# Performance work log

Measured on AMD Instinct MI355X. Metric: run time of the kernel, lower is better.

## Reference

```python
import jax, jax.numpy as jnp
import numpy as np

DEPTH = 4
EPS = 1e-05


def _hard_sigmoid(x):
    # Keras hard_sigmoid: clip(0.2*x + 0.5, 0, 1)
    return jnp.clip(0.2 * x + 0.5, 0.0, 1.0)


def _ln(x, gamma, beta):
    m = jnp.mean(x, axis=-1, keepdims=True)
    std = jnp.sqrt(jnp.var(x, axis=-1, keepdims=True) + EPS)
    return gamma * ((x - m) / (std + EPS)) + beta


def setup_inputs() -> dict:
    key = jax.random.key(0)
    ks = jax.random.split(key, 4)
    B, T, Din, H = 64, 256, 512, 512
    D = Din + H
    O = 2 * H + Din
    x = jax.random.normal(ks[0], (B, T, Din), dtype=jnp.float32)
    mask = jnp.ones((B, T), dtype=bool)
    W = jax.random.normal(ks[1], (D, O), dtype=jnp.float32) * (1.0 / np.sqrt(D))
    U = jax.random.normal(ks[2], (D, O), dtype=jnp.float32) * (1.0 / np.sqrt(D))
    b = jnp.zeros((O,), dtype=jnp.float32)
    gammas = jnp.ones((2, O), dtype=jnp.float32)
    betas = jnp.zeros((2, O), dtype=jnp.float32)
    return {"x": x, "mask": mask, "W": W, "U": U, "b": b,
            "gammas": gammas, "betas": betas, "bucket_size": 256}


def _forward(x, mask, W, U, b, gammas, betas, bucket_size):
    B, T, Din = x.shape
    D = W.shape[0]            # Din + H
    H = W.shape[1] - D        # hidden_dim
    # pad x with zeros in the hidden slots: (B,T,D) -> time-major (Tb,B,D)
    xp = jnp.concatenate([x, jnp.zeros((B, T, H), x.dtype)], axis=-1)
    xs = jnp.transpose(xp, (1, 0, 2))[:bucket_size]           # (Tb,B,D)
    m = jnp.transpose(mask, (1, 0))[:bucket_size]             # (Tb,B) bool
    # mask2 = mask * (1 - shift_left(mask)) : marks the last valid position
    m_shift = jnp.concatenate([m[1:], jnp.zeros((1, B), bool)], axis=0)
    m2 = jnp.logical_and(m, jnp.logical_not(m_shift))          # (Tb,B)
    mf = m.astype(x.dtype)[:, :, None]                         # (Tb,B,1)
    m2f = m2[:, :, None]                                       # (Tb,B,1) bool

    g0, g1 = gammas[0], gammas[1]
    be0, be1 = betas[0], betas[1]

    def hstep(carry, inp):
        h_tm1, fk_tm1 = carry
        xt, fkp, mt, m2t = inp
        sum1 = _ln(xt @ W, g0, be0)
        sum2 = _ln(h_tm1 @ U, g1, be1)
        total = sum1 + sum2 + b
        fk_c = _hard_sigmoid(total[:, :D])                     # (B,D)
        h_ = jnp.tanh(total[:, D:])                            # (B,H)
        h_pad = jnp.concatenate([jnp.zeros((xt.shape[0], D - H), xt.dtype), h_], axis=-1)
        h_cand = (1.0 - fk_c) * xt + fk_c * h_pad
        h = fkp * h_tm1 + (1.0 - fkp) * h_cand
        fk = fkp + (1.0 - fkp) * fk_c
        fk = jnp.where(m2t, 0.0, fk)
        out_h = mt * h + (1.0 - mt) * h_tm1
        out_fk = mt * fk + (1.0 - mt) * fk_tm1
        return (out_h, out_fk), (out_h, out_fk)

    Tb = xs.shape[0]
    fk_prev = jnp.zeros((Tb, B, D), x.dtype)
    h_seq = xs
    for _ in range(DEPTH):
        init = (jnp.zeros((B, D), x.dtype), jnp.zeros((B, D), x.dtype))
        _, (h_seq, fk_seq) = jax.lax.scan(hstep, init, (h_seq, fk_prev, mf, m2f))
        fk_prev = jnp.concatenate([fk_seq[1:], jnp.zeros((1, B, D), x.dtype)], axis=0)
    # outputs = last depth, last timestep, hidden slice
    return h_seq[-1, :, Din:]                                  # (B,H)


def reference(x, mask, W, U, b, gammas, betas, bucket_size):
    return _forward(x, mask, W, U, b, gammas, betas, bucket_size)
```

## Files before the change

### kernel.cpp

```cpp
#include <hip/hip_runtime.h>
#include <hip/hip_bf16.h>
#include <math.h>

#define B_   64
#define T_   256
#define DIN_ 512
#define H_   512
#define D_   1024
#define O_   1536
#define TB_  (T_*B_)
#define EPSf 1e-5f
#define NWG  96
#define NSLOT (T_ + 6)

typedef short  bf16x8 __attribute__((ext_vector_type(8)));
typedef float  f32x4  __attribute__((ext_vector_type(4)));
typedef ushort u16x4  __attribute__((ext_vector_type(4)));
typedef unsigned long long ull;

#define SPLIT1(f, Hm, Lm) { __hip_bfloat16 _h = __float2bfloat16(f); (Hm) = *(ushort*)&_h; \
    __hip_bfloat16 _l = __float2bfloat16((f) - __bfloat162float(_h)); (Lm) = *(ushort*)&_l; }

__device__ inline void st_f32_coh(float* p, float v) {
    __hip_atomic_store(p, v, __ATOMIC_RELAXED, __HIP_MEMORY_SCOPE_AGENT);
}
__device__ inline void st_u16_coh(ushort* p, ushort v) {
    __hip_atomic_store(p, v, __ATOMIC_RELAXED, __HIP_MEMORY_SCOPE_AGENT);
}
__device__ inline void st_u32_coh(unsigned* p, unsigned v) {
    __hip_atomic_store(p, v, __ATOMIC_RELAXED, __HIP_MEMORY_SCOPE_AGENT);
}
__device__ inline void st_f32x2_coh(float* p, float a, float b) {
    union { float f[2]; ull u; } pk;
    pk.f[0] = a; pk.f[1] = b;
    __hip_atomic_store((ull*)p, pk.u, __ATOMIC_RELAXED, __HIP_MEMORY_SCOPE_AGENT);
}

__global__ __launch_bounds__(256) void k_mask(const int* __restrict__ mask,
                                              int* __restrict__ mcode) {
    int g = blockIdx.x * 256 + threadIdx.x;
    int t = g >> 6, b = g & 63;
    int mt = mask[b * T_ + t] != 0;
    int mn = (t + 1 < T_) ? (mask[b * T_ + t + 1] != 0) : 0;
    mcode[g] = mt | (mn << 1);
}

__global__ __launch_bounds__(256) void k_prepx(const float* __restrict__ x,
                                               ushort* __restrict__ Xh) {
    int g  = blockIdx.x * 256 + threadIdx.x;
    int i4 = g * 4;
    int row = i4 >> 10;
    int k   = i4 & 1023;
    int t = row >> 6, b = row & 63;
    float4 v = make_float4(0.f, 0.f, 0.f, 0.f);
    if (k < 512) v = *(const float4*)&x[((size_t)b * T_ + t) * 512 + k];
    u16x4 h;
    __hip_bfloat16 b0 = __float2bfloat16(v.x); h[0] = *(ushort*)&b0;
    __hip_bfloat16 b1 = __float2bfloat16(v.y); h[1] = *(ushort*)&b1;
    __hip_bfloat16 b2 = __float2bfloat16(v.z); h[2] = *(ushort*)&b2;
    __hip_bfloat16 b3 = __float2bfloat16(v.w); h[3] = *(ushort*)&b3;
    *(u16x4*)&Xh[i4] = h;
}

__global__ __launch_bounds__(256) void k_prep(const float* __restrict__ M,
                                              ushort* __restrict__ Mt_hi,
                                              ushort* __restrict__ Mt_lo) {
    __shared__ float ls[64][65];
    int k0 = blockIdx.y * 64;
    int o0 = blockIdx.x * 64;
    int tid = threadIdx.x;
    int r = tid >> 2, cq = tid & 3;
#pragma unroll
    for (int j = 0; j < 4; ++j) {
        float4 v = *(const float4*)&M[(size_t)(k0 + r) * O_ + o0 + cq * 16 + j * 4];
        ls[r][cq * 16 + j * 4 + 0] = v.x;
        ls[r][cq * 16 + j * 4 + 1] = v.y;
        ls[r][cq * 16 + j * 4 + 2] = v.z;
        ls[r][cq * 16 + j * 4 + 3] = v.w;
    }
    __syncthreads();
    int ol = tid >> 2, kq = tid & 3;
    ushort th[16], tl[16];
#pragma unroll
    for (int j = 0; j < 16; ++j) {
        float v = ls[kq * 16 + j][ol];
        SPLIT1(v, th[j], tl[j]);
    }
    size_t base = (size_t)(o0 + ol) * D_ + k0 + kq * 16;
    *(int4*)&Mt_hi[base]     = *(int4*)&th[0];
    *(int4*)&Mt_hi[base + 8] = *(int4*)&th[8];
    *(int4*)&Mt_lo[base]     = *(int4*)&tl[0];
    *(int4*)&Mt_lo[base + 8] = *(int4*)&tl[8];
}

__device__ inline void gbar(unsigned* __restrict__ fl, int w, unsigned bar) {
    __syncthreads();
    asm volatile("s_waitcnt vmcnt(0)" ::: "memory");
    if (threadIdx.x == 0)
        __hip_atomic_store(&fl[w], bar, __ATOMIC_RELAXED, __HIP_MEMORY_SCOPE_AGENT);
    if (threadIdx.x < NWG) {
        while (__hip_atomic_load(&fl[threadIdx.x], __ATOMIC_RELAXED,
                                 __HIP_MEMORY_SCOPE_AGENT) < bar)
            __builtin_amdgcn_s_sleep(2);
    }
    __syncthreads();
    __builtin_amdgcn_fence(__ATOMIC_ACQUIRE, "agent");
}

__global__ __launch_bounds__(256, 1) void k_pipe(
        const float* __restrict__ x,
        const ushort* __restrict__ Xbh,
        ushort* __restrict__ Xrh,
        ushort* __restrict__ Hbh,
        float* __restrict__ Y1, float* __restrict__ Y2,
        float* __restrict__ pstats, float* __restrict__ finals,
        unsigned* __restrict__ ftag, unsigned* __restrict__ flags,
        const ushort* __restrict__ Uth, const ushort* __restrict__ Utl,
        const ushort* __restrict__ Wth, const ushort* __restrict__ Wtl,
        const float* __restrict__ gam, const float* __restrict__ bet,
        const float* __restrict__ bias,
        const int* __restrict__ mcode, float* __restrict__ out) {
    __shared__ __hip_bfloat16 lds[4 * 16 * 1024];
    __shared__ f32x4 ldsc[4][2][64][2];
    const int bx = blockIdx.x;
    const int dom = bx & 1;
    const int w   = bx >> 1;
    const int tid = threadIdx.x;
    const int lane = tid & 63;
    const int wv = tid >> 6;
    const int rt = wv & 1;
    const int kh = wv >> 1;
    const int lr = lane & 15;
    const int lg = lane >> 4;
    const int c0 = w * 16;
    const int br0 = dom * 32 + rt * 16;
    unsigned* fl = flags + dom * 128;
    float* pst   = pstats + (size_t)dom * 4 * 32 * NWG * 4;
    float* fin   = finals + (size_t)dom * 128 * 4;
    unsigned* ft = ftag + (size_t)dom * 128;

    {
        int cl = tid >> 4, kc = tid & 15;
        const ushort* srcs0 = Uth + (size_t)(c0 + cl) * D_ + kc * 64;
        const ushort* srcs1 = Utl + (size_t)(c0 + cl) * D_ + kc * 64;
        const ushort* srcs2 = Wth + (size_t)(c0 + cl) * D_ + kc * 64;
        const ushort* srcs3 = Wtl + (size_t)(c0 + cl) * D_ + kc * 64;
        char* base = (char*)lds;
#pragma unroll
        for (int j = 0; j < 8; ++j) {
            int k = kc * 64 + j * 8;
            int off = (cl * 2048 + k * 2) ^ ((cl & 7) << 4);
            *(int4*)(base + off)           = *(const int4*)(srcs0 + j * 8);
            *(int4*)(base + 32768 + off)   = *(const int4*)(srcs1 + j * 8);
            *(int4*)(base + 65536 + off)   = *(const int4*)(srcs2 + j * 8);
            *(int4*)(base + 98304 + off)   = *(const int4*)(srcs3 + j * 8);
        }
    }
    __syncthreads();

    const int d = c0 + lr;
    const bool gate_w = (w < 64);
    const bool tanh_w = (w >= 32 && w < 64);
    float g0d = 0.f, g1d = 0.f, cd = 0.f, g0e = 0.f, g1e = 0.f, ce = 0.f;
    if (gate_w) {
        g0d = gam[d]; g1d = gam[O_ + d];
        cd  = bet[d] + bet[O_ + d] + bias[d];
    }
    if (tanh_w) {
        int e = d + 512;
        g0e = gam[e]; g1e = gam[O_ + e];
        ce  = bet[e] + bet[O_ + e] + bias[e];
    }

    float h1r[4][4] = {}, fk1r[4][4] = {};
    float oh_d1[4][4] = {}, oh_d2[4][4] = {}, fkp_d1[4][4] = {};
    f32x4 acc1[4], acc2[4];

    unsigned bar = 0;
    for (int s = 0; s < NSLOT; ++s) {
        bool actv[4];
        const ushort* xs[4];
        const ushort* hs[4];
#pragma unroll
        for (int l = 0; l < 4; ++l) {
            int t = s - 2 * l;
            actv[l] = (t >= 0) && (t < T_);
            int tc = t < 0 ? 0 : (t >= T_ ? T_ - 1 : t);
            if (l == 0)
                xs[l] = Xbh + ((size_t)tc * B_ + br0 + lr) * D_ + kh * 512;
            else
                xs[l] = Xrh + (((size_t)l * 3 + (tc % 3)) * B_ + br0 + lr) * D_ + kh * 512;
            hs[l] = Hbh + ((size_t)l * B_ + br0 + lr) * D_ + kh * 512;
        }
        {
            const char* lb = (const char*)lds;
#pragma unroll
            for (int pg = 0; pg < 2; ++pg) {
                f32x4 c1h[2] = {}, c1l[2] = {}, c2h[2] = {}, c2l[2] = {};
#pragma unroll 4
                for (int kc = 0; kc < 16; ++kc) {
                    int kloc = kc * 32 + lg * 8;
                    int kglob = kh * 512 + kloc;
                    int off = (lr * 2048 + kglob * 2) ^ ((lr & 7) << 4);
                    bf16x8 ubh = *(const bf16x8*)(lb + off);
                    bf16x8 ubl = *(const bf16x8*)(lb + 32768 + off);
                    bf16x8 wbh = *(const bf16x8*)(lb + 65536 + off);
                    bf16x8 wbl = *(const bf16x8*)(lb + 98304 + off);
#pragma unroll
                    for (int u = 0; u < 2; ++u) {
                        const int l = pg * 2 + u;
                        bf16x8 xa = *(const bf16x8*)(xs[l] + kloc);
                        bf16x8 ha = *(const bf16x8*)(hs[l] + kloc);
                        c1h[u] = __builtin_amdgcn_mfma_f32_16x16x32_bf16(xa, wbh, c1h[u], 0, 0, 0);
                        c1l[u] = __builtin_amdgcn_mfma_f32_16x16x32_bf16(xa, wbl, c1l[u], 0, 0, 0);
                        c2h[u] = __builtin_amdgcn_mfma_f32_16x16x32_bf16(ha, ubh, c2h[u], 0, 0, 0);
                        c2l[u] = __builtin_amdgcn_mfma_f32_16x16x32_bf16(ha, ubl, c2l[u], 0, 0, 0);
                    }
                }
#pragma unroll
                for (int u = 0; u < 2; ++u) {
                    const int l = pg * 2 + u;
                    acc1[l] = c1h[u] + c1l[u];
                    acc2[l] = c2h[u] + c2l[u];
                }
            }
        }
#pragma unroll
        for (int l = 0; l < 4; ++l) {
            if (actv[l] && kh == 1) {
                ldsc[l][rt][lane][0] = acc1[l];
                ldsc[l][rt][lane][1] = acc2[l];
            }
        }
        __syncthreads();
        if (kh == 0) {
#pragma unroll
            for (int l = 0; l < 4; ++l) {
                if (!actv[l]) continue;
                acc1[l] = acc1[l] + ldsc[l][rt][lane][0];
                acc2[l] = acc2[l] + ldsc[l][rt][lane][1];
#pragma unroll
                for (int j = 0; j < 4; ++j) {
                    float s1 = acc1[l][j], q1 = s1 * s1;
                    float s2 = acc2[l][j], q2 = s2 * s2;
#pragma unroll
                    for (int m = 1; m < 16; m <<= 1) {
                        s1 += __shfl_xor(s1, m); q1 += __shfl_xor(q1, m);
                        s2 += __shfl_xor(s2, m); q2 += __shfl_xor(q2, m);
                    }
                    if (lr == 0) {
                        int lrow = rt * 16 + lg * 4 + j;
                        float* sp = &pst[(((size_t)l * 32 + lrow) * NWG + w) * 4];
                        st_f32x2_coh(sp, s1, q1);
                        st_f32x2_coh(sp + 2, s2, q2);
                    }
                }
                if (w >= 64) {
                    int cexp = c0 + lr - 1024;
#pragma unroll
                    for (int j = 0; j < 4; ++j) {
                        int b = br0 + lg * 4 + j;
                        st_f32_coh(&Y1[((size_t)l * B_ + b) * 512 + cexp], acc1[l][j]);
                        st_f32_coh(&Y2[((size_t)l * B_ + b) * 512 + cexp], acc2[l][j]);
                    }
                }
            }
        }
        gbar(fl, w, ++bar);

        if (wv < 2) {
            int pair = w + NWG * wv;
            if (pair < 128) {
                const float* pp = &pst[(size_t)pair * NWG * 4];
                float s1 = 0.f, q1 = 0.f, s2 = 0.f, q2 = 0.f;
                if (lane < 32) {
#pragma unroll
                    for (int i = 0; i < 3; ++i) {
                        float4 v = *(const float4*)(pp + (lane + i * 32) * 4);
                        s1 += v.x; q1 += v.y; s2 += v.z; q2 += v.w;
                    }
                }
#pragma unroll
                for (int m = 1; m < 32; m <<= 1) {
                    s1 += __shfl_xor(s1, m); q1 += __shfl_xor(q1, m);
                    s2 += __shfl_xor(s2, m); q2 += __shfl_xor(q2, m);
                }
                if (lane == 0) {
                    float m1 = s1 * (1.f / O_);
                    float v1 = q1 * (1.f / O_) - m1 * m1;
                    float i1 = 1.f / (sqrtf(v1 + EPSf) + EPSf);
                    float m2 = s2 * (1.f / O_);
                    float v2 = q2 * (1.f / O_) - m2 * m2;
                    float i2 = 1.f / (sqrtf(v2 + EPSf) + EPSf);
                    st_f32x2_coh(&fin[(size_t)pair * 4], m1, i1);
                    st_f32x2_coh(&fin[(size_t)pair * 4 + 2], m2, i2);
                    asm volatile("s_waitcnt vmcnt(0)" ::: "memory");
                    st_u32_coh(&ft[pair], (unsigned)(s + 1));
                }
            }
        }

        if (gate_w && wv < 2) {
            const int lrow0 = wv * 16 + lg * 4;
            for (;;) {
                bool ready = true;
#pragma unroll
                for (int l = 0; l < 4; ++l) {
                    int t = s - 2 * l;
                    if (t < 0 || t >= T_) continue;
                    unsigned t0 = __hip_atomic_load(&ft[l * 32 + lrow0 + 0], __ATOMIC_RELAXED, __HIP_MEMORY_SCOPE_AGENT);
                    unsigned t1 = __hip_atomic_load(&ft[l * 32 + lrow0 + 1], __ATOMIC_RELAXED, __HIP_MEMORY_SCOPE_AGENT);
                    unsigned t2 = __hip_atomic_load(&ft[l * 32 + lrow0 + 2], __ATOMIC_RELAXED, __HIP_MEMORY_SCOPE_AGENT);
                    unsigned t3 = __hip_atomic_load(&ft[l * 32 + lrow0 + 3], __ATOMIC_RELAXED, __HIP_MEMORY_SCOPE_AGENT);
                    unsigned mn4 = min(min(t0, t1), min(t2, t3));
                    ready = ready && (mn4 >= (unsigned)(s + 1));
                }
                if (ready) break;
                __builtin_amdgcn_s_sleep(1);
            }
#pragma unroll
            for (int li = 0; li < 4; ++li) {
                const int l = 3 - li;
                const int lp = (l > 0) ? l - 1 : 0;
                int t = s - 2 * l;
                bool act = (t >= 0) && (t < T_);
                float ohn[4], ofkn[4];
                if (act) {
                    int b_base = dom * 32 + wv * 16 + lg * 4;
                    int4 mc4 = *(const int4*)&mcode[t * B_ + b_base];
                    int mcarr[4] = {mc4.x, mc4.y, mc4.z, mc4.w};
                    float4 sv[4];
                    float y1e[4], y2e[4];
#pragma unroll
                    for (int j = 0; j < 4; ++j)
                        sv[j] = *(const float4*)&fin[(size_t)(l * 32 + lrow0 + j) * 4];
                    if (tanh_w) {
#pragma unroll
                        for (int j = 0; j < 4; ++j) {
                            int b = b_base + j;
                            y1e[j] = Y1[((size_t)l * B_ + b) * 512 + (d - 512)];
                            y2e[j] = Y2[((size_t)l * B_ + b) * 512 + (d - 512)];
                        }
                    }
#pragma unroll
                    for (int j = 0; j < 4; ++j) {
                        int b = b_base + j;
                        float m1 = sv[j].x, i1 = sv[j].y, m2 = sv[j].z, i2 = sv[j].w;
                        float y1 = acc1[l][j], y2 = acc2[l][j];
                        float td = g0d * (y1 - m1) * i1 + g1d * (y2 - m2) * i2 + cd;
                        float fkc = fminf(fmaxf(0.2f * td + 0.5f, 0.f), 1.f);
                        float hpad = 0.f;
                        if (tanh_w) {
                            float te = g0e * (y1e[j] - m1) * i1 + g1e * (y2e[j] - m2) * i2 + ce;
                            hpad = tanhf(te);
                        }
                        float xt;
                        if (l == 0)
                            xt = (d < 512) ? x[((size_t)b * T_ + t) * 512 + d] : 0.f;
                        else
                            xt = oh_d2[lp][j];
                        float fkp = (l > 0 && t + 1 < T_) ? fkp_d1[lp][j] : 0.f;
                        float hc = (1.f - fkc) * xt + fkc * hpad;
                        float h  = fkp * h1r[l][j] + (1.f - fkp) * hc;
                        float fk = fkp + (1.f - fkp) * fkc;
                        int mt = mcarr[j] & 1, mn = (mcarr[j] >> 1) & 1;
                        if (mt && !mn) fk = 0.f;
                        float oh  = mt ? h  : h1r[l][j];
                        float ofk = mt ? fk : fk1r[l][j];
                        h1r[l][j] = oh; fk1r[l][j] = ofk;
                        __hip_bfloat16 hb = __float2bfloat16(oh);
                        ushort hi = *(ushort*)&hb;
                        st_u16_coh(Hbh + ((size_t)l * B_ + b) * D_ + d, hi);
                        if (l < 3) {
                            size_t xb = (((size_t)(l + 1) * 3 + (t % 3)) * B_ + b) * D_ + d;
                            st_u16_coh(Xrh + xb, hi);
                        }
                        if (l == 3 && t == T_ - 1 && d >= 512)
                            out[(size_t)b * 512 + (d - 512)] = oh;
                        ohn[j] = oh; ofkn[j] = ofk;
                    }
                }
#pragma unroll
                for (int j = 0; j < 4; ++j) {
                    oh_d2[l][j] = oh_d1[l][j];
                    if (act) { oh_d1[l][j] = ohn[j]; fkp_d1[l][j] = ofkn[j]; }
                }
            }
        }
        gbar(fl, w, ++bar);
    }
}

extern "C" void kernel_launch(void* const* d_in, const int* in_sizes, int n_in,
                              void* d_out, int out_size, void* d_ws, size_t ws_size,
                              hipStream_t stream) {
    (void)in_sizes; (void)n_in; (void)out_size;
    const float* x      = (const float*)d_in[0];
    const int*   mask   = (const int*)d_in[1];
    const float* W      = (const float*)d_in[2];
    const float* U      = (const float*)d_in[3];
    const float* bias   = (const float*)d_in[4];
    const float* gammas = (const float*)d_in[5];
    const float* betas  = (const float*)d_in[6];

    float* ws = (float*)d_ws;
    float* Y1    = ws;
    float* Y2    = Y1 + (size_t)4 * B_ * 512;
    float* pstats = Y2 + (size_t)4 * B_ * 512;
    float* finals = pstats + (size_t)2 * 4 * 32 * NWG * 4;
    unsigned* ftag  = (unsigned*)(finals + 2 * 128 * 4);
    unsigned* flags = ftag + 2 * 128;
    int* mcode = (int*)(flags + 256);
    ushort* Xbh = (ushort*)(mcode + TB_);
    ushort* Xrh = Xbh + (size_t)TB_ * D_;
    ushort* Hbh = Xrh + (size_t)4 * 3 * B_ * D_;
    ushort* Uth = Hbh + (size_t)4 * B_ * D_;
    ushort* Utl = Uth + (size_t)O_ * D_;
    ushort* Wth = Utl + (size_t)O_ * D_;
    ushort* Wtl = Wth + (size_t)O_ * D_;
    size_t need_bytes = ((char*)(Wtl + (size_t)O_ * D_)) - ((char*)d_ws);
    if (ws_size < need_bytes) return;

    k_prepx<<<TB_ * D_ / 4 / 256, 256, 0, stream>>>(x, Xbh);
    k_mask<<<TB_ / 256, 256, 0, stream>>>(mask, mcode);
    k_prep<<<dim3(O_ / 64, D_ / 64), 256, 0, stream>>>(U, Uth, Utl);
    k_prep<<<dim3(O_ / 64, D_ / 64), 256, 0, stream>>>(W, Wth, Wtl);
    (void)hipMemsetAsync(Hbh, 0, sizeof(ushort) * (size_t)4 * B_ * D_, stream);
    (void)hipMemsetAsync(pstats, 0, sizeof(float) * (size_t)2 * 4 * 32 * NWG * 4, stream);
    (void)hipMemsetAsync(ftag, 0, sizeof(unsigned) * 2 * 128, stream);
    (void)hipMemsetAsync(flags, 0, sizeof(unsigned) * 256, stream);

    k_pipe<<<2 * NWG, 256, 0, stream>>>(x, Xbh, Xrh, Hbh,
                                        Y1, Y2, pstats, finals, ftag, flags,
                                        Uth, Utl, Wth, Wtl,
                                        gammas, betas, bias, mcode, (float*)d_out);
}
```

Measured before the change: 12.82 ms.

## Split batch into four domains with 128-thread blocks, stream low-part weights from global

Repartitions the persistent pipelined kernel from 2 batch domains of 192 blocks x 256 threads to 4 domains of 384 blocks x 128 threads, each handling 16 batch rows. This halves per-block LDS by keeping only the high bf16 halves of U and W in shared memory and loading the low halves directly from global (L2) each step. The intent is to use more CUs and shorten each block's serial per-step work. In exchange it adds more blocks in each grid barrier and more global/L2 traffic for the weight low parts.

```diff
diff --git a/kernel.cpp b/kernel.cpp
--- a/kernel.cpp
+++ b/kernel.cpp
@@ -11,6 +11,7 @@
 #define TB_  (T_*B_)
 #define EPSf 1e-5f
 #define NWG  96
+#define NDOM 4
 #define NSLOT (T_ + 6)
 
 typedef short  bf16x8 __attribute__((ext_vector_type(8)));
@@ -107,7 +108,7 @@
     __builtin_amdgcn_fence(__ATOMIC_ACQUIRE, "agent");
 }
 
-__global__ __launch_bounds__(256, 1) void k_pipe(
+__global__ __launch_bounds__(128, 1) void k_pipe(
         const float* __restrict__ x,
         const ushort* __restrict__ Xbh,
         ushort* __restrict__ Xrh,
@@ -120,40 +121,34 @@
         const float* __restrict__ gam, const float* __restrict__ bet,
         const float* __restrict__ bias,
         const int* __restrict__ mcode, float* __restrict__ out) {
-    __shared__ __hip_bfloat16 lds[4 * 16 * 1024];
-    __shared__ f32x4 ldsc[4][2][64][2];
+    __shared__ __hip_bfloat16 lds[2 * 16 * 1024];
+    __shared__ f32x4 ldsc[4][64][2];
     const int bx = blockIdx.x;
-    const int dom = bx & 1;
-    const int w   = bx >> 1;
+    const int dom = bx / NWG;
+    const int w   = bx % NWG;
     const int tid = threadIdx.x;
     const int lane = tid & 63;
-    const int wv = tid >> 6;
-    const int rt = wv & 1;
-    const int kh = wv >> 1;
+    const int kh = tid >> 6;
     const int lr = lane & 15;
     const int lg = lane >> 4;
     const int c0 = w * 16;
-    const int br0 = dom * 32 + rt * 16;
+    const int br0 = dom * 16;
     unsigned* fl = flags + dom * 128;
-    float* pst   = pstats + (size_t)dom * 4 * 32 * NWG * 4;
-    float* fin   = finals + (size_t)dom * 128 * 4;
-    unsigned* ft = ftag + (size_t)dom * 128;
+    float* pst   = pstats + (size_t)dom * 64 * NWG * 4;
+    float* fin   = finals + (size_t)dom * 64 * 4;
+    unsigned* ft = ftag + (size_t)dom * 64;
 
     {
-        int cl = tid >> 4, kc = tid & 15;
-        const ushort* srcs0 = Uth + (size_t)(c0 + cl) * D_ + kc * 64;
-        const ushort* srcs1 = Utl + (size_t)(c0 + cl) * D_ + kc * 64;
-        const ushort* srcs2 = Wth + (size_t)(c0 + cl) * D_ + kc * 64;
-        const ushort* srcs3 = Wtl + (size_t)(c0 + cl) * D_ + kc * 64;
+        int cl = tid >> 3, kc = tid & 7;
+        const ushort* s0 = Uth + (size_t)(c0 + cl) * D_ + kc * 128;
+        const ushort* s1 = Wth + (size_t)(c0 + cl) * D_ + kc * 128;
         char* base = (char*)lds;
 #pragma unroll
-        for (int j = 0; j < 8; ++j) {
-            int k = kc * 64 + j * 8;
+        for (int j = 0; j < 16; ++j) {
+            int k = kc * 128 + j * 8;
             int off = (cl * 2048 + k * 2) ^ ((cl & 7) << 4);
-            *(int4*)(base + off)           = *(const int4*)(srcs0 + j * 8);
-            *(int4*)(base + 32768 + off)   = *(const int4*)(srcs1 + j * 8);
-            *(int4*)(base + 65536 + off)   = *(const int4*)(srcs2 + j * 8);
-            *(int4*)(base + 98304 + off)   = *(const int4*)(srcs3 + j * 8);
+            *(int4*)(base + off)         = *(const int4*)(s0 + j * 8);
+            *(int4*)(base + 32768 + off) = *(const int4*)(s1 + j * 8);
         }
     }
     __syncthreads();
@@ -175,6 +170,9 @@
     float h1r[4][4] = {}, fk1r[4][4] = {};
     float oh_d1[4][4] = {}, oh_d2[4][4] = {}, fkp_d1[4][4] = {};
     f32x4 acc1[4], acc2[4];
+
+    const ushort* ulo = Utl + (size_t)(c0 + lr) * D_ + kh * 512;
+    const ushort* wlo = Wtl + (size_t)(c0 + lr) * D_ + kh * 512;
 
     unsigned bar = 0;
     for (int s = 0; s < NSLOT; ++s) {
@@ -203,9 +201,9 @@
                     int kglob = kh * 512 + kloc;
                     int off = (lr * 2048 + kglob * 2) ^ ((lr & 7) << 4);
                     bf16x8 ubh = *(const bf16x8*)(lb + off);
-                    bf16x8 ubl = *(const bf16x8*)(lb + 32768 + off);
-                    bf16x8 wbh = *(const bf16x8*)(lb + 65536 + off);
-                    bf16x8 wbl = *(const bf16x8*)(lb + 98304 + off);
+                    bf16x8 wbh = *(const bf16x8*)(lb + 32768 + off);
+                    bf16x8 ubl = *(const bf16x8*)(ulo + kloc);
+                    bf16x8 wbl = *(const bf16x8*)(wlo + kloc);
 #pragma unroll
                     for (int u = 0; u < 2; ++u) {
                         const int l = pg * 2 + u;
@@ -228,8 +226,8 @@
 #pragma unroll
         for (int l = 0; l < 4; ++l) {
             if (actv[l] && kh == 1) {
-                ldsc[l][rt][lane][0] = acc1[l];
-                ldsc[l][rt][lane][1] = acc2[l];
+                ldsc[l][lane][0] = acc1[l];
+                ldsc[l][lane][1] = acc2[l];
             }
         }
         __syncthreads();
@@ -237,8 +235,8 @@
 #pragma unroll
             for (int l = 0; l < 4; ++l) {
                 if (!actv[l]) continue;
-                acc1[l] = acc1[l] + ldsc[l][rt][lane][0];
-                acc2[l] = acc2[l] + ldsc[l][rt][lane][1];
+                acc1[l] = acc1[l] + ldsc[l][lane][0];
+                acc2[l] = acc2[l] + ldsc[l][lane][1];
 #pragma unroll
                 for (int j = 0; j < 4; ++j) {
                     float s1 = acc1[l][j], q1 = s1 * s1;
@@ -249,8 +247,8 @@
                         s2 += __shfl_xor(s2, m); q2 += __shfl_xor(q2, m);
                     }
                     if (lr == 0) {
-                        int lrow = rt * 16 + lg * 4 + j;
-                        float* sp = &pst[(((size_t)l * 32 + lrow) * NWG + w) * 4];
+                        int lrow = lg * 4 + j;
+                        float* sp = &pst[(((size_t)l * 16 + lrow) * NWG + w) * 4];
                         st_f32x2_coh(sp, s1, q1);
                         st_f32x2_coh(sp + 2, s2, q2);
                     }
@@ -268,50 +266,48 @@
         }
         gbar(fl, w, ++bar);
 
-        if (wv < 2) {
-            int pair = w + NWG * wv;
-            if (pair < 128) {
-                const float* pp = &pst[(size_t)pair * NWG * 4];
-                float s1 = 0.f, q1 = 0.f, s2 = 0.f, q2 = 0.f;
-                if (lane < 32) {
-#pragma unroll
-                    for (int i = 0; i < 3; ++i) {
-                        float4 v = *(const float4*)(pp + (lane + i * 32) * 4);
-                        s1 += v.x; q1 += v.y; s2 += v.z; q2 += v.w;
-                    }
-                }
-#pragma unroll
-                for (int m = 1; m < 32; m <<= 1) {
-                    s1 += __shfl_xor(s1, m); q1 += __shfl_xor(q1, m);
-                    s2 += __shfl_xor(s2, m); q2 += __shfl_xor(q2, m);
-                }
-                if (lane == 0) {
-                    float m1 = s1 * (1.f / O_);
-                    float v1 = q1 * (1.f / O_) - m1 * m1;
-                    float i1 = 1.f / (sqrtf(v1 + EPSf) + EPSf);
-                    float m2 = s2 * (1.f / O_);
-                    float v2 = q2 * (1.f / O_) - m2 * m2;
-                    float i2 = 1.f / (sqrtf(v2 + EPSf) + EPSf);
-                    st_f32x2_coh(&fin[(size_t)pair * 4], m1, i1);
-                    st_f32x2_coh(&fin[(size_t)pair * 4 + 2], m2, i2);
-                    asm volatile("s_waitcnt vmcnt(0)" ::: "memory");
-                    st_u32_coh(&ft[pair], (unsigned)(s + 1));
-                }
-            }
-        }
-
-        if (gate_w && wv < 2) {
-            const int lrow0 = wv * 16 + lg * 4;
+        if (kh == 1 && w < 64) {
+            int pair = w;
+            const float* pp = &pst[(size_t)pair * NWG * 4];
+            float s1 = 0.f, q1 = 0.f, s2 = 0.f, q2 = 0.f;
+            if (lane < 32) {
+#pragma unroll
+                for (int i = 0; i < 3; ++i) {
+                    float4 v = *(const float4*)(pp + (lane + i * 32) * 4);
+                    s1 += v.x; q1 += v.y; s2 += v.z; q2 += v.w;
+                }
+            }
+#pragma unroll
+            for (int m = 1; m < 32; m <<= 1) {
+                s1 += __shfl_xor(s1, m); q1 += __shfl_xor(q1, m);
+                s2 += __shfl_xor(s2, m); q2 += __shfl_xor(q2, m);
+            }
+            if (lane == 0) {
+                float m1 = s1 * (1.f / O_);
+                float v1 = q1 * (1.f / O_) - m1 * m1;
+                float i1 = 1.f / (sqrtf(v1 + EPSf) + EPSf);
+                float m2 = s2 * (1.f / O_);
+                float v2 = q2 * (1.f / O_) - m2 * m2;
+                float i2 = 1.f / (sqrtf(v2 + EPSf) + EPSf);
+                st_f32x2_coh(&fin[(size_t)pair * 4], m1, i1);
+                st_f32x2_coh(&fin[(size_t)pair * 4 + 2], m2, i2);
+                asm volatile("s_waitcnt vmcnt(0)" ::: "memory");
+                st_u32_coh(&ft[pair], (unsigned)(s + 1));
+            }
+        }
+
+        if (kh == 0 && gate_w) {
+            const int lrow0 = lg * 4;
             for (;;) {
                 bool ready = true;
 #pragma unroll
                 for (int l = 0; l < 4; ++l) {
                     int t = s - 2 * l;
                     if (t < 0 || t >= T_) continue;
-                    unsigned t0 = __hip_atomic_load(&ft[l * 32 + lrow0 + 0], __ATOMIC_RELAXED, __HIP_MEMORY_SCOPE_AGENT);
-                    unsigned t1 = __hip_atomic_load(&ft[l * 32 + lrow0 + 1], __ATOMIC_RELAXED, __HIP_MEMORY_SCOPE_AGENT);
-                    unsigned t2 = __hip_atomic_load(&ft[l * 32 + lrow0 + 2], __ATOMIC_RELAXED, __HIP_MEMORY_SCOPE_AGENT);
-                    unsigned t3 = __hip_atomic_load(&ft[l * 32 + lrow0 + 3], __ATOMIC_RELAXED, __HIP_MEMORY_SCOPE_AGENT);
+                    unsigned t0 = __hip_atomic_load(&ft[l * 16 + lrow0 + 0], __ATOMIC_RELAXED, __HIP_MEMORY_SCOPE_AGENT);
+                    unsigned t1 = __hip_atomic_load(&ft[l * 16 + lrow0 + 1], __ATOMIC_RELAXED, __HIP_MEMORY_SCOPE_AGENT);
+                    unsigned t2 = __hip_atomic_load(&ft[l * 16 + lrow0 + 2], __ATOMIC_RELAXED, __HIP_MEMORY_SCOPE_AGENT);
+                    unsigned t3 = __hip_atomic_load(&ft[l * 16 + lrow0 + 3], __ATOMIC_RELAXED, __HIP_MEMORY_SCOPE_AGENT);
                     unsigned mn4 = min(min(t0, t1), min(t2, t3));
                     ready = ready && (mn4 >= (unsigned)(s + 1));
                 }
@@ -326,14 +322,14 @@
                 bool act = (t >= 0) && (t < T_);
                 float ohn[4], ofkn[4];
                 if (act) {
-                    int b_base = dom * 32 + wv * 16 + lg * 4;
+                    int b_base = br0 + lg * 4;
                     int4 mc4 = *(const int4*)&mcode[t * B_ + b_base];
                     int mcarr[4] = {mc4.x, mc4.y, mc4.z, mc4.w};
                     float4 sv[4];
                     float y1e[4], y2e[4];
 #pragma unroll
                     for (int j = 0; j < 4; ++j)
-                        sv[j] = *(const float4*)&fin[(size_t)(l * 32 + lrow0 + j) * 4];
+                        sv[j] = *(const float4*)&fin[(size_t)(l * 16 + lrow0 + j) * 4];
                     if (tanh_w) {
 #pragma unroll
                         for (int j = 0; j < 4; ++j) {
@@ -407,10 +403,10 @@
     float* Y1    = ws;
     float* Y2    = Y1 + (size_t)4 * B_ * 512;
     float* pstats = Y2 + (size_t)4 * B_ * 512;
-    float* finals = pstats + (size_t)2 * 4 * 32 * NWG * 4;
-    unsigned* ftag  = (unsigned*)(finals + 2 * 128 * 4);
-    unsigned* flags = ftag + 2 * 128;
-    int* mcode = (int*)(flags + 256);
+    float* finals = pstats + (size_t)NDOM * 64 * NWG * 4;
+    unsigned* ftag  = (unsigned*)(finals + NDOM * 64 * 4);
+    unsigned* flags = ftag + NDOM * 64;
+    int* mcode = (int*)(flags + NDOM * 128);
     ushort* Xbh = (ushort*)(mcode + TB_);
     ushort* Xrh = Xbh + (size_t)TB_ * D_;
     ushort* Hbh = Xrh + (size_t)4 * 3 * B_ * D_;
@@ -426,12 +422,12 @@
     k_prep<<<dim3(O_ / 64, D_ / 64), 256, 0, stream>>>(U, Uth, Utl);
     k_prep<<<dim3(O_ / 64, D_ / 64), 256, 0, stream>>>(W, Wth, Wtl);
     (void)hipMemsetAsync(Hbh, 0, sizeof(ushort) * (size_t)4 * B_ * D_, stream);
-    (void)hipMemsetAsync(pstats, 0, sizeof(float) * (size_t)2 * 4 * 32 * NWG * 4, stream);
-    (void)hipMemsetAsync(ftag, 0, sizeof(unsigned) * 2 * 128, stream);
-    (void)hipMemsetAsync(flags, 0, sizeof(unsigned) * 256, stream);
-
-    k_pipe<<<2 * NWG, 256, 0, stream>>>(x, Xbh, Xrh, Hbh,
-                                        Y1, Y2, pstats, finals, ftag, flags,
-                                        Uth, Utl, Wth, Wtl,
-                                        gammas, betas, bias, mcode, (float*)d_out);
-}
+    (void)hipMemsetAsync(pstats, 0, sizeof(float) * (size_t)NDOM * 64 * NWG * 4, stream);
+    (void)hipMemsetAsync(ftag, 0, sizeof(unsigned) * NDOM * 64, stream);
+    (void)hipMemsetAsync(flags, 0, sizeof(unsigned) * NDOM * 128, stream);
+
+    k_pipe<<<NDOM * NWG, 128, 0, stream>>>(x, Xbh, Xrh, Hbh,
+                                           Y1, Y2, pstats, finals, ftag, flags,
+                                           Uth, Utl, Wth, Wtl,
+                                           gammas, betas, bias, mcode, (float*)d_out);
+}
```

New measurement: 15.18 ms. 18.4% more time.
